# Performance work log

Measured on AMD Instinct MI355X. Metric: run time of the kernel, lower is better.

Reference implementation:

```python
import jax, jax.numpy as jnp
import numpy as np

OUT, IN, GS = 8192, 8192, 128
N_GROUPS = OUT * IN // GS  # 524288


def setup_inputs() -> dict:
    key = jax.random.key(0)
    k1, k2, k3 = jax.random.split(key, 3)
    x = jax.random.normal(k1, (32, IN), dtype=jnp.float32)
    # ternary values in {-1, 0, 1}
    ternary = jax.random.randint(k2, (OUT, IN), -1, 2, dtype=jnp.int32)
    # positive per-group scales
    scales = jax.random.uniform(k3, (N_GROUPS,), dtype=jnp.float32, minval=0.01, maxval=0.1)
    return {"x": x, "ternary": ternary, "scales": scales}


def reference(x, ternary, scales):
    # Dequantize: each contiguous group of GS weights shares one scale.
    # scales: [n_groups] -> [n_groups, GS] -> [OUT, IN]
    scales_exp = jnp.broadcast_to(scales[:, None], (N_GROUPS, GS)).reshape(OUT, IN)
    w = ternary.astype(jnp.float32) * scales_exp  # [OUT, IN]
    # F.linear(x, w) = x @ w.T
    return jnp.einsum("ti,oi->to", x, w)
```

## Files before the change

### kernel.cpp

```cpp
#include <hip/hip_runtime.h>
#include <hip/hip_bf16.h>
#include <stdint.h>

#define OUT_DIM 8192
#define IN_DIM  8192
#define GS      128
#define MROWS   32
#define NSPLIT  8
#define PART_ELEMS (MROWS * OUT_DIM)

typedef __attribute__((ext_vector_type(8))) short bf16x8;
typedef __attribute__((ext_vector_type(4))) float f32x4;
typedef __attribute__((ext_vector_type(8))) unsigned short u16x8;

__device__ __forceinline__ unsigned short f2bf_rne(float f) {
    uint32_t v = __builtin_bit_cast(uint32_t, f);
    v += 0x7FFFu + ((v >> 16) & 1u);
    return (unsigned short)(v >> 16);
}

__global__ __launch_bounds__(256) void prep_xbf(const float* __restrict__ x,
                                                unsigned short* __restrict__ xbf) {
    int i = (blockIdx.x * 256 + threadIdx.x) * 8;
    float4 a = *(const float4*)(x + i);
    float4 b = *(const float4*)(x + i + 4);
    float f[8] = {a.x, a.y, a.z, a.w, b.x, b.y, b.z, b.w};
    u16x8 u;
#pragma unroll
    for (int j = 0; j < 8; ++j) u[j] = f2bf_rne(f[j]);
    *(u16x8*)(xbf + i) = u;
}

__global__ __launch_bounds__(256) void ternary_gemm(
    const int* __restrict__ tern, const float* __restrict__ scales,
    const unsigned short* __restrict__ xbf, float* __restrict__ part) {
    const int wave  = blockIdx.x * 4 + (threadIdx.x >> 6);
    const int lane  = threadIdx.x & 63;
    const int kc    = wave >> 9;
    const int ntile = wave & 511;
    const int n     = lane & 15;
    const int quad  = lane >> 4;
    const int o      = (ntile << 4) + n;
    const int k0base = kc << 10;

    const int* __restrict__ wrow = tern + (size_t)o * IN_DIM;
    const unsigned short* __restrict__ xr0 = xbf + n * IN_DIM;
    const unsigned short* __restrict__ xr1 = xbf + (16 + n) * IN_DIM;

    const float* __restrict__ sp = scales + o * (IN_DIM / GS) + (kc << 3);
    float s_cur = sp[0];

    f32x4 acc0 = {0.f, 0.f, 0.f, 0.f};
    f32x4 acc1 = {0.f, 0.f, 0.f, 0.f};

#pragma unroll 1
    for (int it = 0; it < 8; ++it) {
        const unsigned int p = f2bf_rne(s_cur);
        float s_nxt = sp[(it < 7) ? (it + 1) : 7];
        const int k0 = k0base + (it << 7);
#pragma unroll
        for (int st = 0; st < 4; ++st) {
            const int k = k0 + (st << 5) + (quad << 3);
            int4 w0 = *(const int4*)(wrow + k);
            int4 w1 = *(const int4*)(wrow + k + 4);
            bf16x8 a0 = *(const bf16x8*)(xr0 + k);
            bf16x8 a1 = *(const bf16x8*)(xr1 + k);
            int tw[8] = {w0.x, w0.y, w0.z, w0.w, w1.x, w1.y, w1.z, w1.w};
            bf16x8 bfr;
#pragma unroll
            for (int j = 0; j < 8; ++j) {
                int t = tw[j];
                unsigned int v = p | ((unsigned int)t & 0x8000u);
                bfr[j] = (short)((t == 0) ? 0u : v);
            }
            acc0 = __builtin_amdgcn_mfma_f32_16x16x32_bf16(a0, bfr, acc0, 0, 0, 0);
            acc1 = __builtin_amdgcn_mfma_f32_16x16x32_bf16(a1, bfr, acc1, 0, 0, 0);
        }
        s_cur = s_nxt;
    }

    float* __restrict__ prow = part + (size_t)kc * PART_ELEMS;
#pragma unroll
    for (int r = 0; r < 4; ++r) {
        prow[(quad * 4 + r) * OUT_DIM + o]        = acc0[r];
        prow[(quad * 4 + r + 16) * OUT_DIM + o]   = acc1[r];
    }
}

__global__ __launch_bounds__(256) void reduce_parts(const float* __restrict__ part,
                                                    float* __restrict__ out) {
    const int i = (blockIdx.x * 256 + threadIdx.x) * 4;
    float4 s = *(const float4*)(part + i);
#pragma unroll
    for (int kc = 1; kc < NSPLIT; ++kc) {
        float4 v = *(const float4*)(part + (size_t)kc * PART_ELEMS + i);
        s.x += v.x; s.y += v.y; s.z += v.z; s.w += v.w;
    }
    *(float4*)(out + i) = s;
}

extern "C" void kernel_launch(void* const* d_in, const int* in_sizes, int n_in,
                              void* d_out, int out_size, void* d_ws, size_t ws_size,
                              hipStream_t stream) {
    const float* x      = (const float*)d_in[0];
    const int*   tern   = (const int*)d_in[1];
    const float* scales = (const float*)d_in[2];
    float* out = (float*)d_out;

    unsigned short* xbf = (unsigned short*)d_ws;
    float* part = (float*)((char*)d_ws + (512 << 10));

    prep_xbf<<<128, 256, 0, stream>>>(x, xbf);
    ternary_gemm<<<1024, 256, 0, stream>>>(tern, scales, xbf, part);
    reduce_parts<<<256, 256, 0, stream>>>(part, out);
}
```

Before: 380.5 us.

## Double-buffer ternary/x loads and use packed perm-multiply dequant

Restructures the GEMM main loop into a software-pipelined ping-pong: the loads for the next 64-wide K slice are issued before the current slice is converted and fed to MFMA. Ternary-to-bf16 conversion now packs two ints per 32-bit register with v_perm and builds the signed scale with an OR and a packed 16-bit multiply instead of per-element selects. It also sets launch_bounds occupancy to 4 blocks per CU and simplifies the output addressing. The added prefetch registers raise register pressure, which could limit occupancy.

```diff
diff --git a/kernel.cpp b/kernel.cpp
--- a/kernel.cpp
+++ b/kernel.cpp
@@ -1,5 +1,4 @@
 #include <hip/hip_runtime.h>
-#include <hip/hip_bf16.h>
 #include <stdint.h>
 
 #define OUT_DIM 8192
@@ -12,6 +11,8 @@
 typedef __attribute__((ext_vector_type(8))) short bf16x8;
 typedef __attribute__((ext_vector_type(4))) float f32x4;
 typedef __attribute__((ext_vector_type(8))) unsigned short u16x8;
+typedef __attribute__((ext_vector_type(2))) unsigned short u16x2;
+typedef __attribute__((ext_vector_type(4))) unsigned int   u32x4;
 
 __device__ __forceinline__ unsigned short f2bf_rne(float f) {
     uint32_t v = __builtin_bit_cast(uint32_t, f);
@@ -31,7 +32,25 @@
     *(u16x8*)(xbf + i) = u;
 }
 
-__global__ __launch_bounds__(256) void ternary_gemm(
+__device__ __forceinline__ unsigned int cvt2(int t0, int t1, unsigned int p32) {
+    unsigned int t16 = __builtin_amdgcn_perm((unsigned int)t1, (unsigned int)t0,
+                                             0x05040100u);
+    unsigned int v   = p32 | (t16 & 0x80008000u);
+    u16x2 r = __builtin_bit_cast(u16x2, v) *
+              __builtin_bit_cast(u16x2, t16 & 0x00010001u);
+    return __builtin_bit_cast(unsigned int, r);
+}
+
+__device__ __forceinline__ bf16x8 conv8(const int4 wa, const int4 wb, unsigned int p32) {
+    u32x4 d;
+    d[0] = cvt2(wa.x, wa.y, p32);
+    d[1] = cvt2(wa.z, wa.w, p32);
+    d[2] = cvt2(wb.x, wb.y, p32);
+    d[3] = cvt2(wb.z, wb.w, p32);
+    return __builtin_bit_cast(bf16x8, d);
+}
+
+__global__ __launch_bounds__(256, 4) void ternary_gemm(
     const int* __restrict__ tern, const float* __restrict__ scales,
     const unsigned short* __restrict__ xbf, float* __restrict__ part) {
     const int wave  = blockIdx.x * 4 + (threadIdx.x >> 6);
@@ -40,50 +59,73 @@
     const int ntile = wave & 511;
     const int n     = lane & 15;
     const int quad  = lane >> 4;
-    const int o      = (ntile << 4) + n;
-    const int k0base = kc << 10;
+    const int o     = (ntile << 4) + n;
+    const int kbase = (kc << 10) + (quad << 3);
 
-    const int* __restrict__ wrow = tern + (size_t)o * IN_DIM;
-    const unsigned short* __restrict__ xr0 = xbf + n * IN_DIM;
-    const unsigned short* __restrict__ xr1 = xbf + (16 + n) * IN_DIM;
-
-    const float* __restrict__ sp = scales + o * (IN_DIM / GS) + (kc << 3);
-    float s_cur = sp[0];
+    const int* __restrict__ wrow            = tern + (size_t)o * IN_DIM + kbase;
+    const unsigned short* __restrict__ xr0  = xbf + n * IN_DIM + kbase;
+    const unsigned short* __restrict__ xr1  = xbf + (16 + n) * IN_DIM + kbase;
+    const float* __restrict__ sp            = scales + o * (IN_DIM / GS) + (kc << 3);
 
     f32x4 acc0 = {0.f, 0.f, 0.f, 0.f};
     f32x4 acc1 = {0.f, 0.f, 0.f, 0.f};
 
+    int4   wa0, wa1, wa2, wa3, wb0, wb1, wb2, wb3;
+    bf16x8 xa0, xa1, xa2, xa3, xb0, xb1, xb2, xb3;
+
+#define LOADA(IT) do { const int kk = (IT) << 6;                              \
+        wa0 = *(const int4*)(wrow + kk);       wa1 = *(const int4*)(wrow + kk + 4);  \
+        wa2 = *(const int4*)(wrow + kk + 32);  wa3 = *(const int4*)(wrow + kk + 36); \
+        xa0 = *(const bf16x8*)(xr0 + kk);      xa1 = *(const bf16x8*)(xr0 + kk + 32);\
+        xa2 = *(const bf16x8*)(xr1 + kk);      xa3 = *(const bf16x8*)(xr1 + kk + 32);\
+    } while (0)
+#define LOADB(IT) do { const int kk = (IT) << 6;                              \
+        wb0 = *(const int4*)(wrow + kk);       wb1 = *(const int4*)(wrow + kk + 4);  \
+        wb2 = *(const int4*)(wrow + kk + 32);  wb3 = *(const int4*)(wrow + kk + 36); \
+        xb0 = *(const bf16x8*)(xr0 + kk);      xb1 = *(const bf16x8*)(xr0 + kk + 32);\
+        xb2 = *(const bf16x8*)(xr1 + kk);      xb3 = *(const bf16x8*)(xr1 + kk + 32);\
+    } while (0)
+#define CONSA(P) do {                                                         \
+        bf16x8 f0 = conv8(wa0, wa1, (P));  bf16x8 f1 = conv8(wa2, wa3, (P));  \
+        acc0 = __builtin_amdgcn_mfma_f32_16x16x32_bf16(xa0, f0, acc0, 0, 0, 0);\
+        acc1 = __builtin_amdgcn_mfma_f32_16x16x32_bf16(xa2, f0, acc1, 0, 0, 0);\
+        acc0 = __builtin_amdgcn_mfma_f32_16x16x32_bf16(xa1, f1, acc0, 0, 0, 0);\
+        acc1 = __builtin_amdgcn_mfma_f32_16x16x32_bf16(xa3, f1, acc1, 0, 0, 0);\
+    } while (0)
+#define CONSB(P) do {                                                         \
+        bf16x8 f0 = conv8(wb0, wb1, (P));  bf16x8 f1 = conv8(wb2, wb3, (P));  \
+        acc0 = __builtin_amdgcn_mfma_f32_16x16x32_bf16(xb0, f0, acc0, 0, 0, 0);\
+        acc1 = __builtin_amdgcn_mfma_f32_16x16x32_bf16(xb2, f0, acc1, 0, 0, 0);\
+        acc0 = __builtin_amdgcn_mfma_f32_16x16x32_bf16(xb1, f1, acc0, 0, 0, 0);\
+        acc1 = __builtin_amdgcn_mfma_f32_16x16x32_bf16(xb3, f1, acc1, 0, 0, 0);\
+    } while (0)
+
+    LOADA(0);
+    float s_cur = sp[0];
+
 #pragma unroll 1
-    for (int it = 0; it < 8; ++it) {
-        const unsigned int p = f2bf_rne(s_cur);
-        float s_nxt = sp[(it < 7) ? (it + 1) : 7];
-        const int k0 = k0base + (it << 7);
-#pragma unroll
-        for (int st = 0; st < 4; ++st) {
-            const int k = k0 + (st << 5) + (quad << 3);
-            int4 w0 = *(const int4*)(wrow + k);
-            int4 w1 = *(const int4*)(wrow + k + 4);
-            bf16x8 a0 = *(const bf16x8*)(xr0 + k);
-            bf16x8 a1 = *(const bf16x8*)(xr1 + k);
-            int tw[8] = {w0.x, w0.y, w0.z, w0.w, w1.x, w1.y, w1.z, w1.w};
-            bf16x8 bfr;
-#pragma unroll
-            for (int j = 0; j < 8; ++j) {
-                int t = tw[j];
-                unsigned int v = p | ((unsigned int)t & 0x8000u);
-                bfr[j] = (short)((t == 0) ? 0u : v);
-            }
-            acc0 = __builtin_amdgcn_mfma_f32_16x16x32_bf16(a0, bfr, acc0, 0, 0, 0);
-            acc1 = __builtin_amdgcn_mfma_f32_16x16x32_bf16(a1, bfr, acc1, 0, 0, 0);
-        }
+    for (int pr = 0; pr < 8; ++pr) {
+        const int it1 = (pr << 1) + 1;
+        LOADB(it1);
+        float s_nxt = sp[(pr < 7) ? (pr + 1) : 7];
+        const unsigned int ph  = f2bf_rne(s_cur);
+        const unsigned int p32 = ph | (ph << 16);
+        CONSA(p32);
+        LOADA((pr < 7) ? (it1 + 1) : 15);
+        CONSB(p32);
         s_cur = s_nxt;
     }
+#undef LOADA
+#undef LOADB
+#undef CONSA
+#undef CONSB
 
-    float* __restrict__ prow = part + (size_t)kc * PART_ELEMS;
+    float* __restrict__ prow = part + (size_t)kc * PART_ELEMS
+                             + (size_t)(quad << 2) * OUT_DIM + o;
 #pragma unroll
     for (int r = 0; r < 4; ++r) {
-        prow[(quad * 4 + r) * OUT_DIM + o]        = acc0[r];
-        prow[(quad * 4 + r + 16) * OUT_DIM + o]   = acc1[r];
+        prow[(size_t)r * OUT_DIM]        = acc0[r];
+        prow[(size_t)(r + 16) * OUT_DIM] = acc1[r];
     }
 }
 
```

Result: slower. 408.2 us (+7.3%).

## Stage ternary weight tiles through double-buffered LDS with coalesced loads

Applied to the files above, without the earlier changes.

Each block now handles a 64-output by 1024-K tile. It loads the int32 ternary weights cooperatively: 16 threads cover each row's contiguous 256 bytes, replacing the scattered per-lane row reads that strided across 8192-int rows. Tiles go into a double-buffered LDS array, and the next K-slice is prefetched into registers while the current slice is converted and fed to MFMA. The intent is better-coalesced DRAM traffic for the dominant weight stream, plus overlap of loads with compute. The cost is an extra LDS round-trip, about 35KB of LDS per block, and a barrier every 64-K stage.

```diff
diff --git a/kernel.cpp b/kernel.cpp
--- a/kernel.cpp
+++ b/kernel.cpp
@@ -1,5 +1,4 @@
 #include <hip/hip_runtime.h>
-#include <hip/hip_bf16.h>
 #include <stdint.h>
 
 #define OUT_DIM 8192
@@ -7,6 +6,9 @@
 #define GS      128
 #define MROWS   32
 #define NSPLIT  8
+#define KCHUNK  1024
+#define KS      64
+#define NSTG    (KCHUNK / KS)
 #define PART_ELEMS (MROWS * OUT_DIM)
 
 typedef __attribute__((ext_vector_type(8))) short bf16x8;
@@ -34,37 +36,69 @@
 __global__ __launch_bounds__(256) void ternary_gemm(
     const int* __restrict__ tern, const float* __restrict__ scales,
     const unsigned short* __restrict__ xbf, float* __restrict__ part) {
-    const int wave  = blockIdx.x * 4 + (threadIdx.x >> 6);
-    const int lane  = threadIdx.x & 63;
-    const int kc    = wave >> 9;
-    const int ntile = wave & 511;
-    const int n     = lane & 15;
-    const int quad  = lane >> 4;
-    const int o      = (ntile << 4) + n;
-    const int k0base = kc << 10;
+    __shared__ __align__(16) int lds_w[2][64][68];
 
-    const int* __restrict__ wrow = tern + (size_t)o * IN_DIM;
-    const unsigned short* __restrict__ xr0 = xbf + n * IN_DIM;
-    const unsigned short* __restrict__ xr1 = xbf + (16 + n) * IN_DIM;
+    const int tid  = threadIdx.x;
+    const int wv   = tid >> 6;
+    const int lane = tid & 63;
+    const int n    = lane & 15;
+    const int quad = lane >> 4;
 
+    const int otile = blockIdx.x & 127;
+    const int kc    = blockIdx.x >> 7;
+    const int o0    = otile << 6;
+    const int o     = o0 + (wv << 4) + n;
+    const int kpos0 = kc << 10;
+
+    const int srow = tid >> 4;
+    const int scol = (tid & 15) << 2;
+    const int* __restrict__ wbase = tern + (size_t)o0 * IN_DIM + kpos0 + scol;
+
+    const unsigned short* __restrict__ xr0 = xbf + n * IN_DIM + kpos0 + (quad << 3);
+    const unsigned short* __restrict__ xr1 = xbf + (16 + n) * IN_DIM + kpos0 + (quad << 3);
     const float* __restrict__ sp = scales + o * (IN_DIM / GS) + (kc << 3);
-    float s_cur = sp[0];
 
     f32x4 acc0 = {0.f, 0.f, 0.f, 0.f};
     f32x4 acc1 = {0.f, 0.f, 0.f, 0.f};
 
+    {
+        int4 s0 = *(const int4*)(wbase + (size_t)srow * IN_DIM);
+        int4 s1 = *(const int4*)(wbase + (size_t)(16 + srow) * IN_DIM);
+        int4 s2 = *(const int4*)(wbase + (size_t)(32 + srow) * IN_DIM);
+        int4 s3 = *(const int4*)(wbase + (size_t)(48 + srow) * IN_DIM);
+        *(int4*)&lds_w[0][srow][scol]      = s0;
+        *(int4*)&lds_w[0][16 + srow][scol] = s1;
+        *(int4*)&lds_w[0][32 + srow][scol] = s2;
+        *(int4*)&lds_w[0][48 + srow][scol] = s3;
+    }
+    __syncthreads();
+
+    float s_nxt = sp[0];
+
 #pragma unroll 1
-    for (int it = 0; it < 8; ++it) {
-        const unsigned int p = f2bf_rne(s_cur);
-        float s_nxt = sp[(it < 7) ? (it + 1) : 7];
-        const int k0 = k0base + (it << 7);
+    for (int stg = 0; stg < NSTG; ++stg) {
+        const int buf = stg & 1;
+        int4 s0, s1, s2, s3;
+        if (stg < NSTG - 1) {
+            const int* __restrict__ wb = wbase + (stg + 1) * KS;
+            s0 = *(const int4*)(wb + (size_t)srow * IN_DIM);
+            s1 = *(const int4*)(wb + (size_t)(16 + srow) * IN_DIM);
+            s2 = *(const int4*)(wb + (size_t)(32 + srow) * IN_DIM);
+            s3 = *(const int4*)(wb + (size_t)(48 + srow) * IN_DIM);
+        }
+        const float s_use  = s_nxt;
+        const float s_pref = sp[(stg < NSTG - 1) ? ((stg + 1) >> 1) : 7];
+        const unsigned int p = f2bf_rne(s_use);
+
+        const int kk0  = stg * KS;
+        const int lrow = (wv << 4) + n;
 #pragma unroll
-        for (int st = 0; st < 4; ++st) {
-            const int k = k0 + (st << 5) + (quad << 3);
-            int4 w0 = *(const int4*)(wrow + k);
-            int4 w1 = *(const int4*)(wrow + k + 4);
-            bf16x8 a0 = *(const bf16x8*)(xr0 + k);
-            bf16x8 a1 = *(const bf16x8*)(xr1 + k);
+        for (int half = 0; half < 2; ++half) {
+            const int kk = half << 5;
+            int4 w0 = *(const int4*)&lds_w[buf][lrow][kk + (quad << 3)];
+            int4 w1 = *(const int4*)&lds_w[buf][lrow][kk + (quad << 3) + 4];
+            bf16x8 a0 = *(const bf16x8*)(xr0 + kk0 + kk);
+            bf16x8 a1 = *(const bf16x8*)(xr1 + kk0 + kk);
             int tw[8] = {w0.x, w0.y, w0.z, w0.w, w1.x, w1.y, w1.z, w1.w};
             bf16x8 bfr;
 #pragma unroll
@@ -76,14 +110,21 @@
             acc0 = __builtin_amdgcn_mfma_f32_16x16x32_bf16(a0, bfr, acc0, 0, 0, 0);
             acc1 = __builtin_amdgcn_mfma_f32_16x16x32_bf16(a1, bfr, acc1, 0, 0, 0);
         }
-        s_cur = s_nxt;
+        if (stg < NSTG - 1) {
+            *(int4*)&lds_w[buf ^ 1][srow][scol]      = s0;
+            *(int4*)&lds_w[buf ^ 1][16 + srow][scol] = s1;
+            *(int4*)&lds_w[buf ^ 1][32 + srow][scol] = s2;
+            *(int4*)&lds_w[buf ^ 1][48 + srow][scol] = s3;
+        }
+        __syncthreads();
+        s_nxt = s_pref;
     }
 
     float* __restrict__ prow = part + (size_t)kc * PART_ELEMS;
 #pragma unroll
     for (int r = 0; r < 4; ++r) {
-        prow[(quad * 4 + r) * OUT_DIM + o]        = acc0[r];
-        prow[(quad * 4 + r + 16) * OUT_DIM + o]   = acc1[r];
+        prow[(quad * 4 + r) * OUT_DIM + o]      = acc0[r];
+        prow[(quad * 4 + r + 16) * OUT_DIM + o] = acc1[r];
     }
 }
 
@@ -111,6 +152,6 @@
     float* part = (float*)((char*)d_ws + (512 << 10));
 
     prep_xbf<<<128, 256, 0, stream>>>(x, xbf);
-    ternary_gemm<<<1024, 256, 0, stream>>>(tern, scales, xbf, part);
+    ternary_gemm<<<128 * NSPLIT, 256, 0, stream>>>(tern, scales, xbf, part);
     reduce_parts<<<256, 256, 0, stream>>>(part, out);
 }
```

Result: slower. 408.5 us (+7.3%).

## Pre-compress ternary weights to bytes and decode with byte-permute in GEMM

Applied to the files above, without the earlier changes.

Adds a pre-pass that packs each int32 ternary weight into one byte holding its sign and nonzero bits. The GEMM then reads a quarter of the weight bytes and decodes pairs into bf16 using perm and packed 16-bit multiply instead of per-element selects. This adds an extra kernel that still streams the full int32 weights every call and writes the packed copy, trading extra total traffic for a lighter, less latency-bound main loop.

```diff
diff --git a/kernel.cpp b/kernel.cpp
--- a/kernel.cpp
+++ b/kernel.cpp
@@ -1,5 +1,4 @@
 #include <hip/hip_runtime.h>
-#include <hip/hip_bf16.h>
 #include <stdint.h>
 
 #define OUT_DIM 8192
@@ -12,6 +11,8 @@
 typedef __attribute__((ext_vector_type(8))) short bf16x8;
 typedef __attribute__((ext_vector_type(4))) float f32x4;
 typedef __attribute__((ext_vector_type(8))) unsigned short u16x8;
+typedef __attribute__((ext_vector_type(2))) unsigned short u16x2;
+typedef __attribute__((ext_vector_type(4))) unsigned int   u32x4;
 
 __device__ __forceinline__ unsigned short f2bf_rne(float f) {
     uint32_t v = __builtin_bit_cast(uint32_t, f);
@@ -31,8 +32,43 @@
     *(u16x8*)(xbf + i) = u;
 }
 
+__global__ __launch_bounds__(256) void compress_w(const int* __restrict__ t,
+                                                  unsigned int* __restrict__ c) {
+    const size_t base = (size_t)blockIdx.x * 4096;
+    const int tid = threadIdx.x;
+#pragma unroll
+    for (int j = 0; j < 4; ++j) {
+        const size_t ii = base + (size_t)(j << 10) + (size_t)(tid << 2);
+        int4 w = *(const int4*)(t + ii);
+        unsigned int r = ((unsigned int)w.x & 0x81u)
+                       | (((unsigned int)w.y & 0x81u) << 8)
+                       | (((unsigned int)w.z & 0x81u) << 16)
+                       | (((unsigned int)w.w & 0x81u) << 24);
+        c[ii >> 2] = r;
+    }
+}
+
+__device__ __forceinline__ unsigned int cvt2b(unsigned int dw, unsigned int p32,
+                                              unsigned int ssel, unsigned int asel) {
+    unsigned int s16 = __builtin_amdgcn_perm(0u, dw, ssel);
+    unsigned int a16 = __builtin_amdgcn_perm(0u, dw, asel);
+    unsigned int v   = p32 | (s16 & 0x80008000u);
+    u16x2 r = __builtin_bit_cast(u16x2, v) *
+              __builtin_bit_cast(u16x2, a16 & 0x00010001u);
+    return __builtin_bit_cast(unsigned int, r);
+}
+
+__device__ __forceinline__ bf16x8 conv8b(uint2 dw, unsigned int p32) {
+    u32x4 d;
+    d[0] = cvt2b(dw.x, p32, 0x01040004u, 0x04010400u);
+    d[1] = cvt2b(dw.x, p32, 0x03040204u, 0x04030402u);
+    d[2] = cvt2b(dw.y, p32, 0x01040004u, 0x04010400u);
+    d[3] = cvt2b(dw.y, p32, 0x03040204u, 0x04030402u);
+    return __builtin_bit_cast(bf16x8, d);
+}
+
 __global__ __launch_bounds__(256) void ternary_gemm(
-    const int* __restrict__ tern, const float* __restrict__ scales,
+    const unsigned char* __restrict__ comp, const float* __restrict__ scales,
     const unsigned short* __restrict__ xbf, float* __restrict__ part) {
     const int wave  = blockIdx.x * 4 + (threadIdx.x >> 6);
     const int lane  = threadIdx.x & 63;
@@ -43,9 +79,9 @@
     const int o      = (ntile << 4) + n;
     const int k0base = kc << 10;
 
-    const int* __restrict__ wrow = tern + (size_t)o * IN_DIM;
-    const unsigned short* __restrict__ xr0 = xbf + n * IN_DIM;
-    const unsigned short* __restrict__ xr1 = xbf + (16 + n) * IN_DIM;
+    const unsigned char*  __restrict__ wrow = comp + (size_t)o * IN_DIM;
+    const unsigned short* __restrict__ xr0  = xbf + n * IN_DIM;
+    const unsigned short* __restrict__ xr1  = xbf + (16 + n) * IN_DIM;
 
     const float* __restrict__ sp = scales + o * (IN_DIM / GS) + (kc << 3);
     float s_cur = sp[0];
@@ -55,24 +91,17 @@
 
 #pragma unroll 1
     for (int it = 0; it < 8; ++it) {
-        const unsigned int p = f2bf_rne(s_cur);
+        const unsigned int ph  = f2bf_rne(s_cur);
+        const unsigned int p32 = ph | (ph << 16);
         float s_nxt = sp[(it < 7) ? (it + 1) : 7];
         const int k0 = k0base + (it << 7);
 #pragma unroll
         for (int st = 0; st < 4; ++st) {
             const int k = k0 + (st << 5) + (quad << 3);
-            int4 w0 = *(const int4*)(wrow + k);
-            int4 w1 = *(const int4*)(wrow + k + 4);
+            uint2 dw = *(const uint2*)(wrow + k);
             bf16x8 a0 = *(const bf16x8*)(xr0 + k);
             bf16x8 a1 = *(const bf16x8*)(xr1 + k);
-            int tw[8] = {w0.x, w0.y, w0.z, w0.w, w1.x, w1.y, w1.z, w1.w};
-            bf16x8 bfr;
-#pragma unroll
-            for (int j = 0; j < 8; ++j) {
-                int t = tw[j];
-                unsigned int v = p | ((unsigned int)t & 0x8000u);
-                bfr[j] = (short)((t == 0) ? 0u : v);
-            }
+            bf16x8 bfr = conv8b(dw, p32);
             acc0 = __builtin_amdgcn_mfma_f32_16x16x32_bf16(a0, bfr, acc0, 0, 0, 0);
             acc1 = __builtin_amdgcn_mfma_f32_16x16x32_bf16(a1, bfr, acc1, 0, 0, 0);
         }
@@ -82,8 +111,8 @@
     float* __restrict__ prow = part + (size_t)kc * PART_ELEMS;
 #pragma unroll
     for (int r = 0; r < 4; ++r) {
-        prow[(quad * 4 + r) * OUT_DIM + o]        = acc0[r];
-        prow[(quad * 4 + r + 16) * OUT_DIM + o]   = acc1[r];
+        prow[(quad * 4 + r) * OUT_DIM + o]      = acc0[r];
+        prow[(quad * 4 + r + 16) * OUT_DIM + o] = acc1[r];
     }
 }
 
@@ -107,10 +136,13 @@
     const float* scales = (const float*)d_in[2];
     float* out = (float*)d_out;
 
-    unsigned short* xbf = (unsigned short*)d_ws;
-    float* part = (float*)((char*)d_ws + (512 << 10));
+    unsigned short* xbf  = (unsigned short*)d_ws;
+    float*          part = (float*)((char*)d_ws + (512 << 10));
+    unsigned int*   comp = (unsigned int*)((char*)d_ws + (16u << 20));
 
+    compress_w<<<(OUT_DIM * (IN_DIM / 4096)), 256, 0, stream>>>(tern, comp);
     prep_xbf<<<128, 256, 0, stream>>>(x, xbf);
-    ternary_gemm<<<1024, 256, 0, stream>>>(tern, scales, xbf, part);
+    ternary_gemm<<<1024, 256, 0, stream>>>((const unsigned char*)comp, scales,
+                                           xbf, part);
     reduce_parts<<<256, 256, 0, stream>>>(part, out);
 }
```

Measured after the change: 417.1 us. 1.1x slower.
